# Optimization experiments

Measured on AMD Instinct MI355X. Metric: run time of the kernel, lower is better.

The kernel has to match this reference:

```python
import jax, jax.numpy as jnp
import numpy as np

E = 8      # num_experts
D = 512    # input feature dim
H1 = 512   # expert_hidden[0]
H2 = 256   # expert_hidden[1]
Y = 256    # y_dim
B = 8192   # batch
ALPHA = 0.2


def setup_inputs() -> dict:
    key = jax.random.key(0)
    ks = jax.random.split(key, 8)
    h = jax.random.normal(ks[0], (B, D), dtype=jnp.float32)
    gate_id = jax.random.randint(ks[1], (B,), 0, E, dtype=jnp.int64)
    # Per-expert MLP parameters, stacked over expert axis (Glorot-ish scale)
    W1 = jax.random.normal(ks[2], (E, D, H1), dtype=jnp.float32) * (1.0 / np.sqrt(D))
    b1 = jnp.zeros((E, H1), dtype=jnp.float32)
    W2 = jax.random.normal(ks[3], (E, H1, H2), dtype=jnp.float32) * (1.0 / np.sqrt(H1))
    b2 = jnp.zeros((E, H2), dtype=jnp.float32)
    W3 = jax.random.normal(ks[4], (E, H2, Y), dtype=jnp.float32) * (1.0 / np.sqrt(H2))
    b3 = jnp.zeros((E, Y), dtype=jnp.float32)
    return {"h": h, "gate_id": gate_id, "W1": W1, "b1": b1,
            "W2": W2, "b2": b2, "W3": W3, "b3": b3}


def _leaky(x):
    return jnp.where(x > 0, x, ALPHA * x)


def reference(h, gate_id, W1, b1, W2, b2, W3, b3):
    # Hard routing: gate_id = clip(round(gate_id), 0, E-1)
    g = jnp.clip(jnp.round(gate_id.astype(jnp.float32)).astype(jnp.int32), 0, E - 1)
    # Dense all-experts compute (jit-friendly, no dynamic shapes), then select
    # the routed expert's output per row. Same math as dispatch/stitch.
    a1 = _leaky(jnp.einsum('bd,edh->ebh', h, W1) + b1[:, None, :])   # [E,B,H1]
    a2 = _leaky(jnp.einsum('ebh,ehk->ebk', a1, W2) + b2[:, None, :]) # [E,B,H2]
    y = jnp.einsum('ebk,eky->eby', a2, W3) + b3[:, None, :]          # [E,B,Y]
    out = y[g, jnp.arange(h.shape[0])]                                # [B,Y]
    return out
```

## Files before the change

### kernel.cpp

```cpp
#include <hip/hip_runtime.h>
#include <stdint.h>

#define NE 8
#define ND 512
#define NH1 512
#define NH2 256
#define NY 256
#define NB 8192
#define BM3 32
#define MAXT3 (NB/BM3 + NE - 1)
#define W1T64 (NE * (ND/64) * (NH1/64))
#define W2T64 (NE * (NH1/64) * (NH2/64))
#define W3T64 (NE * (NH2/64) * (NY/64))
#define WTT64 (W1T64 + W2T64 + W3T64)

typedef float f32x4 __attribute__((ext_vector_type(4)));
typedef __bf16 bf16x8 __attribute__((ext_vector_type(8)));
typedef unsigned short u16x8 __attribute__((ext_vector_type(8)));

__device__ __forceinline__ unsigned short f2bf(float f) {
  unsigned int u = __float_as_uint(f);
  u += 0x7fffu + ((u >> 16) & 1u);
  return (unsigned short)(u >> 16);
}

__device__ __forceinline__ int clampe(int g) {
  return g < 0 ? 0 : (g > NE - 1 ? NE - 1 : g);
}



__global__ __launch_bounds__(256)
void prep_k(const int* __restrict__ gate,
            const float* __restrict__ W1, const float* __restrict__ W2,
            const float* __restrict__ W3,
            unsigned short* __restrict__ w1f, unsigned short* __restrict__ w2f,
            unsigned short* __restrict__ w3f,
            int* __restrict__ meta, int* __restrict__ perm)
{
  __shared__ char sm[17024] __attribute__((aligned(16)));
  int b = blockIdx.x, t = threadIdx.x;

  if (b < WTT64) {
    float* ldsf = (float*)sm;
    const float* src; unsigned short* dst; int K, N, idx;
    if (b < W1T64)          { src = W1; dst = w1f; K = ND;  N = NH1; idx = b; }
    else if (b < W1T64 + W2T64) { src = W2; dst = w2f; K = NH1; N = NH2; idx = b - W1T64; }
    else                    { src = W3; dst = w3f; K = NH2; N = NY;  idx = b - W1T64 - W2T64; }
    int ntn = N >> 6, ntk = K >> 6;
    int n0 = (idx % ntn) * 64;
    int k0 = ((idx / ntn) % ntk) * 64;
    int g  = idx / (ntn * ntk);

    {
      int r  = t >> 2;
      int c4 = t & 3;
      const float* s = src + (size_t)g * K * N + (size_t)(k0 + r) * N + n0;
      #pragma unroll
      for (int i = 0; i < 4; i++) {
        float4 v = *(const float4*)(s + (i * 4 + c4) * 4);
        *(float4*)(ldsf + r * 65 + (i * 4 + c4) * 4) = v;
      }
    }
    __syncthreads();

    unsigned short* d = dst + (size_t)g * K * N;
    #pragma unroll
    for (int ii = 0; ii < 2; ii++) {
      int idx2 = ii * 256 + t;
      int lane = idx2 & 63;
      int f    = (idx2 >> 6) & 3;
      int kt   = idx2 >> 8;
      int kl   = kt * 32 + (lane >> 4) * 8;
      int nl   = f * 16 + (lane & 15);
      union { u16x8 v; unsigned short u[8]; } pk;
      #pragma unroll
      for (int j = 0; j < 8; j++)
        pk.u[j] = f2bf(ldsf[(kl + j) * 65 + nl]);
      int ktg = (k0 >> 5) + kt;
      int fg  = (n0 >> 4) + f;
      *(u16x8*)(d + (((size_t)ktg * (N >> 4) + fg) * 64 + lane) * 8) = pk.v;
    }
    return;
  }

  unsigned int* lcnt_lo = (unsigned int*)sm;
  unsigned int* lcnt_hi = lcnt_lo + 256;
  int* pre   = (int*)(sm + 2048);
  int* cnt8  = (int*)(sm + 2048 + 8192);
  int* offs8 = cnt8 + 8;

  unsigned int gp[8];
  unsigned int clo = 0, chi = 0;
  #pragma unroll
  for (int i = 0; i < 32; i++) {
    int g = clampe(gate[t * 32 + i]);
    if ((i & 3) == 0) gp[i >> 2] = 0;
    gp[i >> 2] |= (unsigned int)g << (8 * (i & 3));
    if (g < 4) clo += 1u << (8 * g);
    else       chi += 1u << (8 * (g - 4));
  }
  lcnt_lo[t] = clo;
  lcnt_hi[t] = chi;
  __syncthreads();

  int wave = t >> 6, lane = t & 63;
  #pragma unroll
  for (int pass = 0; pass < 2; pass++) {
    int e = wave + pass * 4;
    int carry = 0;
    #pragma unroll
    for (int ch = 0; ch < 4; ch++) {
      int idx = ch * 64 + lane;
      unsigned int word = (e < 4) ? lcnt_lo[idx] : lcnt_hi[idx];
      int v = (int)((word >> (8 * (e & 3))) & 255u);
      int s = v;
      #pragma unroll
      for (int d = 1; d < 64; d <<= 1) {
        int up = __shfl_up(s, d, 64);
        if (lane >= d) s += up;
      }
      pre[e * 256 + idx] = carry + s - v;
      carry += __shfl(s, 63, 64);
    }
    if (lane == 0) cnt8[e] = carry;
  }
  __syncthreads();

  if (t == 0) {
    int off = 0, tt2 = 0;
    for (int e = 0; e < NE; e++) {
      int cc = cnt8[e];
      meta[e] = cc;
      meta[8 + e] = off;
      offs8[e] = off;
      int ntl = (cc + BM3 - 1) / BM3;
      for (int i = 0; i < ntl; i++) meta[1024 + tt2++] = (e << 16) | i;
      off += cc;
    }
    meta[24] = tt2;
  }
  __syncthreads();

  unsigned int rlo = 0, rhi = 0;
  #pragma unroll
  for (int i = 0; i < 32; i++) {
    int g = (int)((gp[i >> 2] >> (8 * (i & 3))) & 255u);
    int r;
    if (g < 4) { r = (int)((rlo >> (8 * g)) & 255u);       rlo += 1u << (8 * g); }
    else       { r = (int)((rhi >> (8 * (g - 4))) & 255u); rhi += 1u << (8 * (g - 4)); }
    perm[offs8[g] + pre[g * 256 + t] + r] = t * 32 + i;
  }
}

__global__ __launch_bounds__(512, 6)
void mlp_k(const float* __restrict__ h,
           const float* __restrict__ b1, const float* __restrict__ b2,
           const float* __restrict__ b3,
           float* __restrict__ out,
           const int* __restrict__ meta, const int* __restrict__ perm,
           const unsigned short* __restrict__ w1f,
           const unsigned short* __restrict__ w2f,
           const unsigned short* __restrict__ w3f)
{
  __shared__ unsigned short sA[BM3 * 520];
  __shared__ unsigned short sB[BM3 * 520];
  __shared__ int permc[BM3];

  if ((int)blockIdx.x >= meta[24]) return;

  int tid  = threadIdx.x;
  int ent  = meta[1024 + blockIdx.x];
  int e    = ent >> 16;
  int trow = ent & 0xffff;
  int cnt  = meta[e];
  int off  = meta[8 + e];
  int row0 = trow * BM3;

  if (tid < BM3) {
    int grow = row0 + tid;
    permc[tid] = (grow < cnt) ? perm[off + grow] : 0;
  }
  __syncthreads();

  int wave = tid >> 6, lane = tid & 63;
  int lm = lane & 15, quad = lane >> 4;

  {
    int r  = tid >> 4;
    int cb = (tid & 15) * 8;
    const float* hrow = h + (size_t)permc[r] * ND;
    #pragma unroll
    for (int jj = 0; jj < 4; jj++) {
      int col = cb + jj * 128;
      float4 f0 = *(const float4*)(hrow + col);
      float4 f1 = *(const float4*)(hrow + col + 4);
      union { u16x8 v; unsigned short u[8]; } pk;
      pk.u[0] = f2bf(f0.x); pk.u[1] = f2bf(f0.y); pk.u[2] = f2bf(f0.z); pk.u[3] = f2bf(f0.w);
      pk.u[4] = f2bf(f1.x); pk.u[5] = f2bf(f1.y); pk.u[6] = f2bf(f1.z); pk.u[7] = f2bf(f1.w);
      *(u16x8*)(sA + r * 520 + col) = pk.v;
    }
  }
  __syncthreads();

  f32x4 zero = {0.f, 0.f, 0.f, 0.f};

  {
    f32x4 acc[2][4];
    #pragma unroll
    for (int mi = 0; mi < 2; mi++)
      #pragma unroll
      for (int ni = 0; ni < 4; ni++)
        acc[mi][ni] = zero;
    const unsigned short* Wb = w1f + (size_t)e * ND * NH1 + ((size_t)(wave * 4) * 64 + lane) * 8;
    bf16x8 cur[4], nxt[4];
    #pragma unroll
    for (int ni = 0; ni < 4; ni++)
      cur[ni] = *reinterpret_cast<const bf16x8*>(Wb + ni * 512);
    for (int t = 0; t < 16; t++) {
      int tn = (t + 1 < 16) ? t + 1 : t;
      #pragma unroll
      for (int ni = 0; ni < 4; ni++)
        nxt[ni] = *reinterpret_cast<const bf16x8*>(Wb + (size_t)tn * 16384 + ni * 512);
      bf16x8 af[2];
      #pragma unroll
      for (int mi = 0; mi < 2; mi++)
        af[mi] = *reinterpret_cast<const bf16x8*>(sA + (mi * 16 + lm) * 520 + t * 32 + quad * 8);
      #pragma unroll
      for (int mi = 0; mi < 2; mi++)
        #pragma unroll
        for (int ni = 0; ni < 4; ni++)
          acc[mi][ni] = __builtin_amdgcn_mfma_f32_16x16x32_bf16(af[mi], cur[ni], acc[mi][ni], 0, 0, 0);
      #pragma unroll
      for (int ni = 0; ni < 4; ni++)
        cur[ni] = nxt[ni];
    }
    #pragma unroll
    for (int mi = 0; mi < 2; mi++)
      #pragma unroll
      for (int ni = 0; ni < 4; ni++) {
        int col = (wave * 4 + ni) * 16 + lm;
        float bv = b1[e * NH1 + col];
        #pragma unroll
        for (int r = 0; r < 4; r++) {
          int row = mi * 16 + quad * 4 + r;
          float v = acc[mi][ni][r] + bv;
          v = (v > 0.f) ? v : 0.2f * v;
          sB[row * 520 + col] = f2bf(v);
        }
      }
  }
  __syncthreads();

  {
    f32x4 acc[2][2];
    #pragma unroll
    for (int mi = 0; mi < 2; mi++)
      #pragma unroll
      for (int ni = 0; ni < 2; ni++)
        acc[mi][ni] = zero;
    const unsigned short* Wb = w2f + (size_t)e * NH1 * NH2 + ((size_t)(wave * 2) * 64 + lane) * 8;
    bf16x8 cur[2], nxt[2];
    #pragma unroll
    for (int ni = 0; ni < 2; ni++)
      cur[ni] = *reinterpret_cast<const bf16x8*>(Wb + ni * 512);
    for (int t = 0; t < 16; t++) {
      int tn = (t + 1 < 16) ? t + 1 : t;
      #pragma unroll
      for (int ni = 0; ni < 2; ni++)
        nxt[ni] = *reinterpret_cast<const bf16x8*>(Wb + (size_t)tn * 8192 + ni * 512);
      bf16x8 af[2];
      #pragma unroll
      for (int mi = 0; mi < 2; mi++)
        af[mi] = *reinterpret_cast<const bf16x8*>(sB + (mi * 16 + lm) * 520 + t * 32 + quad * 8);
      #pragma unroll
      for (int mi = 0; mi < 2; mi++)
        #pragma unroll
        for (int ni = 0; ni < 2; ni++)
          acc[mi][ni] = __builtin_amdgcn_mfma_f32_16x16x32_bf16(af[mi], cur[ni], acc[mi][ni], 0, 0, 0);
      #pragma unroll
      for (int ni = 0; ni < 2; ni++)
        cur[ni] = nxt[ni];
    }
    #pragma unroll
    for (int mi = 0; mi < 2; mi++)
      #pragma unroll
      for (int ni = 0; ni < 2; ni++) {
        int col = (wave * 2 + ni) * 16 + lm;
        float bv = b2[e * NH2 + col];
        #pragma unroll
        for (int r = 0; r < 4; r++) {
          int row = mi * 16 + quad * 4 + r;
          float v = acc[mi][ni][r] + bv;
          v = (v > 0.f) ? v : 0.2f * v;
          sA[row * 264 + col] = f2bf(v);
        }
      }
  }
  __syncthreads();

  {
    f32x4 acc[2][2];
    #pragma unroll
    for (int mi = 0; mi < 2; mi++)
      #pragma unroll
      for (int ni = 0; ni < 2; ni++)
        acc[mi][ni] = zero;
    const unsigned short* Wb = w3f + (size_t)e * NH2 * NY + ((size_t)(wave * 2) * 64 + lane) * 8;
    bf16x8 cur[2], nxt[2];
    #pragma unroll
    for (int ni = 0; ni < 2; ni++)
      cur[ni] = *reinterpret_cast<const bf16x8*>(Wb + ni * 512);
    for (int t = 0; t < 8; t++) {
      int tn = (t + 1 < 8) ? t + 1 : t;
      #pragma unroll
      for (int ni = 0; ni < 2; ni++)
        nxt[ni] = *reinterpret_cast<const bf16x8*>(Wb + (size_t)tn * 8192 + ni * 512);
      bf16x8 af[2];
      #pragma unroll
      for (int mi = 0; mi < 2; mi++)
        af[mi] = *reinterpret_cast<const bf16x8*>(sA + (mi * 16 + lm) * 264 + t * 32 + quad * 8);
      #pragma unroll
      for (int mi = 0; mi < 2; mi++)
        #pragma unroll
        for (int ni = 0; ni < 2; ni++)
          acc[mi][ni] = __builtin_amdgcn_mfma_f32_16x16x32_bf16(af[mi], cur[ni], acc[mi][ni], 0, 0, 0);
      #pragma unroll
      for (int ni = 0; ni < 2; ni++)
        cur[ni] = nxt[ni];
    }
    #pragma unroll
    for (int mi = 0; mi < 2; mi++)
      #pragma unroll
      for (int ni = 0; ni < 2; ni++) {
        int col = (wave * 2 + ni) * 16 + lm;
        float bv = b3[e * NY + col];
        #pragma unroll
        for (int r = 0; r < 4; r++) {
          int row = mi * 16 + quad * 4 + r;
          int grow = row0 + row;
          if (grow < cnt) {
            float v = acc[mi][ni][r] + bv;
            out[(size_t)permc[row] * NY + col] = v;
          }
        }
      }
  }
}

extern "C" void kernel_launch(void* const* d_in, const int* in_sizes, int n_in,
                              void* d_out, int out_size, void* d_ws, size_t ws_size,
                              hipStream_t stream) {
  (void)in_sizes; (void)n_in; (void)out_size; (void)ws_size;
  const float* h  = (const float*)d_in[0];
  const int* gate = (const int*)d_in[1];
  const float* W1 = (const float*)d_in[2];
  const float* b1 = (const float*)d_in[3];
  const float* W2 = (const float*)d_in[4];
  const float* b2 = (const float*)d_in[5];
  const float* W3 = (const float*)d_in[6];
  const float* b3 = (const float*)d_in[7];
  float* out = (float*)d_out;

  char* ws = (char*)d_ws;
  int* meta = (int*)ws;
  int* perm = (int*)(ws + 8192);
  unsigned short* w1f = (unsigned short*)(ws + 8192 + 32768);
  unsigned short* w2f = w1f + (size_t)NE * ND * NH1;
  unsigned short* w3f = w2f + (size_t)NE * NH1 * NH2;

  prep_k<<<WTT64 + 1, 256, 0, stream>>>(gate, W1, W2, W3, w1f, w2f, w3f, meta, perm);
  mlp_k<<<MAXT3, 512, 0, stream>>>(h, b1, b2, b3, out, meta, perm, w1f, w2f, w3f);
}
```

Before: 120.2 us.

## Deepen weight prefetch to 4-stage register ring and prefetch next layer weights

Replaces the single-step weight prefetch in each of the three expert GEMM loops with a 4-deep register ring buffer that loads weights three k-steps ahead. The activation fragments read from LDS are also double-buffered. The first stages of the next layer's weights are issued before the current layer's epilogue, and layer-1 weights before the h gather. Launch bounds are relaxed from 6 to 2 waves per SIMD to give room for the extra registers, trading occupancy for more latency hiding inside each block.

```diff
diff --git a/kernel.cpp b/kernel.cpp
--- a/kernel.cpp
+++ b/kernel.cpp
@@ -51,7 +51,6 @@
     int n0 = (idx % ntn) * 64;
     int k0 = ((idx / ntn) % ntk) * 64;
     int g  = idx / (ntn * ntk);
-
     {
       int r  = t >> 2;
       int c4 = t & 3;
@@ -63,7 +62,6 @@
       }
     }
     __syncthreads();
-
     unsigned short* d = dst + (size_t)g * K * N;
     #pragma unroll
     for (int ii = 0; ii < 2; ii++) {
@@ -153,7 +151,7 @@
   }
 }
 
-__global__ __launch_bounds__(512, 6)
+__global__ __launch_bounds__(512, 2)
 void mlp_k(const float* __restrict__ h,
            const float* __restrict__ b1, const float* __restrict__ b2,
            const float* __restrict__ b3,
@@ -177,14 +175,28 @@
   int off  = meta[8 + e];
   int row0 = trow * BM3;
 
+  int wave = tid >> 6, lane = tid & 63;
+  int lm = lane & 15, quad = lane >> 4;
+
+  const unsigned short* W1b = w1f + (size_t)e * ND * NH1 + ((size_t)(wave * 4) * 64 + lane) * 8;
+  const unsigned short* W2b = w2f + (size_t)e * NH1 * NH2 + ((size_t)(wave * 2) * 64 + lane) * 8;
+  const unsigned short* W3b = w3f + (size_t)e * NH2 * NY + ((size_t)(wave * 2) * 64 + lane) * 8;
+
+  bf16x8 w1s[4][4];
+  bf16x8 w2s[4][2];
+  bf16x8 w3s[4][2];
+
+  #pragma unroll
+  for (int s = 0; s < 3; s++)
+    #pragma unroll
+    for (int ni = 0; ni < 4; ni++)
+      w1s[s][ni] = *reinterpret_cast<const bf16x8*>(W1b + (size_t)s * 16384 + ni * 512);
+
   if (tid < BM3) {
     int grow = row0 + tid;
     permc[tid] = (grow < cnt) ? perm[off + grow] : 0;
   }
   __syncthreads();
-
-  int wave = tid >> 6, lane = tid & 63;
-  int lm = lane & 15, quad = lane >> 4;
 
   {
     int r  = tid >> 4;
@@ -212,29 +224,31 @@
       #pragma unroll
       for (int ni = 0; ni < 4; ni++)
         acc[mi][ni] = zero;
-    const unsigned short* Wb = w1f + (size_t)e * ND * NH1 + ((size_t)(wave * 4) * 64 + lane) * 8;
-    bf16x8 cur[4], nxt[4];
-    #pragma unroll
-    for (int ni = 0; ni < 4; ni++)
-      cur[ni] = *reinterpret_cast<const bf16x8*>(Wb + ni * 512);
+    bf16x8 ast[2][2];
+    #pragma unroll
+    for (int mi = 0; mi < 2; mi++)
+      ast[0][mi] = *reinterpret_cast<const bf16x8*>(sA + (mi * 16 + lm) * 520 + quad * 8);
+    #pragma unroll
     for (int t = 0; t < 16; t++) {
-      int tn = (t + 1 < 16) ? t + 1 : t;
+      int tw = (t + 3 < 16) ? t + 3 : 15;
       #pragma unroll
       for (int ni = 0; ni < 4; ni++)
-        nxt[ni] = *reinterpret_cast<const bf16x8*>(Wb + (size_t)tn * 16384 + ni * 512);
-      bf16x8 af[2];
-      #pragma unroll
-      for (int mi = 0; mi < 2; mi++)
-        af[mi] = *reinterpret_cast<const bf16x8*>(sA + (mi * 16 + lm) * 520 + t * 32 + quad * 8);
+        w1s[(t + 3) & 3][ni] = *reinterpret_cast<const bf16x8*>(W1b + (size_t)tw * 16384 + ni * 512);
+      int ta = (t + 1 < 16) ? t + 1 : 15;
+      #pragma unroll
+      for (int mi = 0; mi < 2; mi++)
+        ast[(t + 1) & 1][mi] = *reinterpret_cast<const bf16x8*>(sA + (mi * 16 + lm) * 520 + ta * 32 + quad * 8);
       #pragma unroll
       for (int mi = 0; mi < 2; mi++)
         #pragma unroll
         for (int ni = 0; ni < 4; ni++)
-          acc[mi][ni] = __builtin_amdgcn_mfma_f32_16x16x32_bf16(af[mi], cur[ni], acc[mi][ni], 0, 0, 0);
-      #pragma unroll
-      for (int ni = 0; ni < 4; ni++)
-        cur[ni] = nxt[ni];
-    }
+          acc[mi][ni] = __builtin_amdgcn_mfma_f32_16x16x32_bf16(ast[t & 1][mi], w1s[t & 3][ni], acc[mi][ni], 0, 0, 0);
+    }
+    #pragma unroll
+    for (int s = 0; s < 3; s++)
+      #pragma unroll
+      for (int ni = 0; ni < 2; ni++)
+        w2s[s][ni] = *reinterpret_cast<const bf16x8*>(W2b + (size_t)s * 8192 + ni * 512);
     #pragma unroll
     for (int mi = 0; mi < 2; mi++)
       #pragma unroll
@@ -259,29 +273,31 @@
       #pragma unroll
       for (int ni = 0; ni < 2; ni++)
         acc[mi][ni] = zero;
-    const unsigned short* Wb = w2f + (size_t)e * NH1 * NH2 + ((size_t)(wave * 2) * 64 + lane) * 8;
-    bf16x8 cur[2], nxt[2];
-    #pragma unroll
-    for (int ni = 0; ni < 2; ni++)
-      cur[ni] = *reinterpret_cast<const bf16x8*>(Wb + ni * 512);
+    bf16x8 ast[2][2];
+    #pragma unroll
+    for (int mi = 0; mi < 2; mi++)
+      ast[0][mi] = *reinterpret_cast<const bf16x8*>(sB + (mi * 16 + lm) * 520 + quad * 8);
+    #pragma unroll
     for (int t = 0; t < 16; t++) {
-      int tn = (t + 1 < 16) ? t + 1 : t;
-      #pragma unroll
-      for (int ni = 0; ni < 2; ni++)
-        nxt[ni] = *reinterpret_cast<const bf16x8*>(Wb + (size_t)tn * 8192 + ni * 512);
-      bf16x8 af[2];
-      #pragma unroll
-      for (int mi = 0; mi < 2; mi++)
-        af[mi] = *reinterpret_cast<const bf16x8*>(sB + (mi * 16 + lm) * 520 + t * 32 + quad * 8);
+      int tw = (t + 3 < 16) ? t + 3 : 15;
+      #pragma unroll
+      for (int ni = 0; ni < 2; ni++)
+        w2s[(t + 3) & 3][ni] = *reinterpret_cast<const bf16x8*>(W2b + (size_t)tw * 8192 + ni * 512);
+      int ta = (t + 1 < 16) ? t + 1 : 15;
+      #pragma unroll
+      for (int mi = 0; mi < 2; mi++)
+        ast[(t + 1) & 1][mi] = *reinterpret_cast<const bf16x8*>(sB + (mi * 16 + lm) * 520 + ta * 32 + quad * 8);
       #pragma unroll
       for (int mi = 0; mi < 2; mi++)
         #pragma unroll
         for (int ni = 0; ni < 2; ni++)
-          acc[mi][ni] = __builtin_amdgcn_mfma_f32_16x16x32_bf16(af[mi], cur[ni], acc[mi][ni], 0, 0, 0);
-      #pragma unroll
-      for (int ni = 0; ni < 2; ni++)
-        cur[ni] = nxt[ni];
-    }
+          acc[mi][ni] = __builtin_amdgcn_mfma_f32_16x16x32_bf16(ast[t & 1][mi], w2s[t & 3][ni], acc[mi][ni], 0, 0, 0);
+    }
+    #pragma unroll
+    for (int s = 0; s < 3; s++)
+      #pragma unroll
+      for (int ni = 0; ni < 2; ni++)
+        w3s[s][ni] = *reinterpret_cast<const bf16x8*>(W3b + (size_t)s * 8192 + ni * 512);
     #pragma unroll
     for (int mi = 0; mi < 2; mi++)
       #pragma unroll
@@ -306,28 +322,25 @@
       #pragma unroll
       for (int ni = 0; ni < 2; ni++)
         acc[mi][ni] = zero;
-    const unsigned short* Wb = w3f + (size_t)e * NH2 * NY + ((size_t)(wave * 2) * 64 + lane) * 8;
-    bf16x8 cur[2], nxt[2];
-    #pragma unroll
-    for (int ni = 0; ni < 2; ni++)
-      cur[ni] = *reinterpret_cast<const bf16x8*>(Wb + ni * 512);
+    bf16x8 ast[2][2];
+    #pragma unroll
+    for (int mi = 0; mi < 2; mi++)
+      ast[0][mi] = *reinterpret_cast<const bf16x8*>(sA + (mi * 16 + lm) * 264 + quad * 8);
+    #pragma unroll
     for (int t = 0; t < 8; t++) {
-      int tn = (t + 1 < 8) ? t + 1 : t;
-      #pragma unroll
-      for (int ni = 0; ni < 2; ni++)
-        nxt[ni] = *reinterpret_cast<const bf16x8*>(Wb + (size_t)tn * 8192 + ni * 512);
-      bf16x8 af[2];
-      #pragma unroll
-      for (int mi = 0; mi < 2; mi++)
-        af[mi] = *reinterpret_cast<const bf16x8*>(sA + (mi * 16 + lm) * 264 + t * 32 + quad * 8);
+      int tw = (t + 3 < 8) ? t + 3 : 7;
+      #pragma unroll
+      for (int ni = 0; ni < 2; ni++)
+        w3s[(t + 3) & 3][ni] = *reinterpret_cast<const bf16x8*>(W3b + (size_t)tw * 8192 + ni * 512);
+      int ta = (t + 1 < 8) ? t + 1 : 7;
+      #pragma unroll
+      for (int mi = 0; mi < 2; mi++)
+        ast[(t + 1) & 1][mi] = *reinterpret_cast<const bf16x8*>(sA + (mi * 16 + lm) * 264 + ta * 32 + quad * 8);
       #pragma unroll
       for (int mi = 0; mi < 2; mi++)
         #pragma unroll
         for (int ni = 0; ni < 2; ni++)
-          acc[mi][ni] = __builtin_amdgcn_mfma_f32_16x16x32_bf16(af[mi], cur[ni], acc[mi][ni], 0, 0, 0);
-      #pragma unroll
-      for (int ni = 0; ni < 2; ni++)
-        cur[ni] = nxt[ni];
+          acc[mi][ni] = __builtin_amdgcn_mfma_f32_16x16x32_bf16(ast[t & 1][mi], w3s[t & 3][ni], acc[mi][ni], 0, 0, 0);
     }
     #pragma unroll
     for (int mi = 0; mi < 2; mi++)
```

Result: slower. 131.0 us (+8.9%).
